# Optimization experiments

Measured on AMD Instinct MI355X. Metric: run time of the kernel, lower is better.

## Reference

```python
import jax, jax.numpy as jnp
import numpy as np

TOP_K = 2


def setup_inputs() -> dict:
    key = jax.random.key(0)
    ks = jax.random.split(key, 8)
    B, S, H, I, E = 1, 1024, 2048, 1408, 8
    s = 0.02  # init scale for weights
    return {
        "hidden_states": jax.random.normal(ks[0], (B, S, H), jnp.float32),
        "gate_weight": jax.random.normal(ks[1], (E, H), jnp.float32) * s,
        "expert_gate_w": jax.random.normal(ks[2], (E, I, H), jnp.float32) * s,
        "expert_up_w": jax.random.normal(ks[3], (E, I, H), jnp.float32) * s,
        "expert_down_w": jax.random.normal(ks[4], (E, H, I), jnp.float32) * s,
        "shared_gate_w": jax.random.normal(ks[5], (I, H), jnp.float32) * s,
        "shared_up_w": jax.random.normal(ks[6], (I, H), jnp.float32) * s,
        "shared_down_w": jax.random.normal(ks[7], (H, I), jnp.float32) * s,
    }


def reference(hidden_states, gate_weight, expert_gate_w, expert_up_w, expert_down_w,
              shared_gate_w, shared_up_w, shared_down_w):
    B, S, H = hidden_states.shape
    E = gate_weight.shape[0]
    x = hidden_states.reshape(-1, H)          # [T, H]
    T = x.shape[0]

    # --- gate: top-k routing (e_score_correction_bias buffer is zeros -> no-op) ---
    logits = x @ gate_weight.T                # [T, E]
    topk_logits, topk_idx = jax.lax.top_k(logits, TOP_K)
    topk_w = jax.nn.softmax(topk_logits, axis=-1)  # [T, K]

    # per-token per-expert combine weight (0 for non-selected experts) [T, E]
    comb = jnp.zeros((T, E), x.dtype).at[jnp.arange(T)[:, None], topk_idx].add(topk_w)

    # --- routed experts: dense over E, weighted combine (mathematically identical
    # to the per-token loop since comb==0 for unselected experts) ---
    g = jnp.einsum('th,eih->tei', x, expert_gate_w)   # [T, E, I]
    u = jnp.einsum('th,eih->tei', x, expert_up_w)     # [T, E, I]
    h = jax.nn.silu(g) * u                            # [T, E, I]
    y = jnp.einsum('tei,ehi->teh', h, expert_down_w)  # [T, E, H]
    out = jnp.einsum('teh,te->th', y, comb)           # [T, H]

    # --- shared expert ---
    sh = (jax.nn.silu(x @ shared_gate_w.T) * (x @ shared_up_w.T)) @ shared_down_w.T
    out = out + sh
    return out.reshape(B, S, H)
```

## Files before the change

### kernel.cpp

```cpp
#include <hip/hip_runtime.h>
#include <hip/hip_bf16.h>

typedef unsigned short u16;
typedef __bf16 bf16x8 __attribute__((ext_vector_type(8)));
typedef float f32x4 __attribute__((ext_vector_type(4)));

#define H_DIM 2048
#define I_DIM 1408
#define T_TOK 1024
#define NEXP 8
#define LS 40

__device__ __forceinline__ u16 f2bf(float f) {
    union { float f; unsigned u; } v; v.f = f;
    unsigned r = v.u + 0x7FFFu + ((v.u >> 16) & 1u);
    return (u16)(r >> 16);
}
__device__ __forceinline__ unsigned pack2(float a, float b) {
    float2 t; t.x = a; t.y = b;
    __hip_bfloat162 h = __float22bfloat162_rn(t);
    union { __hip_bfloat162 h; unsigned u; } v; v.h = h;
    return v.u;
}
__device__ __forceinline__ uint2 pack4(float4 f) {
    uint2 r; r.x = pack2(f.x, f.y); r.y = pack2(f.z, f.w); return r;
}
__device__ __forceinline__ void g2l16(const void* g, void* l) {
    __builtin_amdgcn_global_load_lds((const __attribute__((address_space(1))) void*)g,
                                     (__attribute__((address_space(3))) void*)l, 16, 0, 0);
}

__global__ __launch_bounds__(256)
void router_kernel(const float* __restrict__ x, const float* __restrict__ gw,
                   int* __restrict__ counts, int* __restrict__ tok, float* __restrict__ tw) {
    int wave = threadIdx.x >> 6;
    int lane = threadIdx.x & 63;
    int t = blockIdx.x * 4 + wave;
    const float* xr = x + (size_t)t * H_DIM;
    float acc[NEXP];
#pragma unroll
    for (int e = 0; e < NEXP; e++) acc[e] = 0.f;
    for (int h = lane; h < H_DIM; h += 64) {
        float xv = xr[h];
#pragma unroll
        for (int e = 0; e < NEXP; e++) acc[e] += xv * gw[e * H_DIM + h];
    }
#pragma unroll
    for (int e = 0; e < NEXP; e++) {
#pragma unroll
        for (int off = 32; off > 0; off >>= 1) acc[e] += __shfl_xor(acc[e], off);
    }
    if (lane == 0) {
        int i0 = 0; float v0 = acc[0];
#pragma unroll
        for (int e = 1; e < NEXP; e++) if (acc[e] > v0) { v0 = acc[e]; i0 = e; }
        int i1 = -1; float v1 = -3.0e38f;
#pragma unroll
        for (int e = 0; e < NEXP; e++) if (e != i0 && acc[e] > v1) { v1 = acc[e]; i1 = e; }
        float ex = __expf(v1 - v0);
        float w0 = 1.f / (1.f + ex);
        float w1 = 1.f - w0;
        int s0 = atomicAdd(&counts[i0], 1);
        tok[i0 * T_TOK + s0] = t; tw[i0 * T_TOK + s0] = w0;
        int s1 = atomicAdd(&counts[i1], 1);
        tok[i1 * T_TOK + s1] = t; tw[i1 * T_TOK + s1] = w1;
    }
}

struct Cvt7 { const float* in[7]; u16* out[7]; int nchunk[7]; };
__global__ __launch_bounds__(256)
void convert_bf(Cvt7 a) {
    int z = blockIdx.z;
    int n = a.nchunk[z];
    const float* in = a.in[z]; u16* out = a.out[z];
    for (int i = blockIdx.x * 256 + threadIdx.x; i < n; i += gridDim.x * 256) {
        const float4* p = (const float4*)(in + (size_t)i * 8);
        float4 f0 = p[0], f1 = p[1];
        uint4 o; o.x = pack2(f0.x, f0.y); o.y = pack2(f0.z, f0.w);
        o.z = pack2(f1.x, f1.y); o.w = pack2(f1.z, f1.w);
        *(uint4*)(out + (size_t)i * 8) = o;
    }
}

__global__ __launch_bounds__(256, 3)
void gate_up_bf(const u16* __restrict__ xb,
                const u16* __restrict__ egw, const u16* __restrict__ euw,
                const u16* __restrict__ sgw, const u16* __restrict__ suw,
                const int* __restrict__ counts, const int* __restrict__ tok,
                const float* __restrict__ tw,
                u16* __restrict__ h_r, u16* __restrict__ h_s) {
    __shared__ u16 lA[64 * 64];
    __shared__ u16 lG[128 * 64];
    __shared__ u16 lU[128 * 64];

    int e = blockIdx.z;
    bool routed = (e < NEXP);
    int cnt, hbase; const u16 *Wg, *Wu; u16* hout;
    if (routed) {
        cnt = counts[e];
        int p = 0;
#pragma unroll
        for (int i = 0; i < NEXP; i++) { int c = counts[i]; if (i < e) p += c; }
        hbase = p;
        Wg = egw + (size_t)e * I_DIM * H_DIM;
        Wu = euw + (size_t)e * I_DIM * H_DIM;
        hout = h_r;
    } else { cnt = T_TOK; hbase = 0; Wg = sgw; Wu = suw; hout = h_s; }
    int m0 = blockIdx.y * 64;
    if (m0 >= cnt) return;
    int n0 = blockIdx.x * 128;

    int tid = threadIdx.x, lane = tid & 63, w = tid >> 6;

    const u16* aptr[2]; u16* alds[2];
#pragma unroll
    for (int j = 0; j < 2; j++) {
        int chunk = w * 128 + j * 64 + lane;
        int row = chunk >> 3, cl = chunk & 7;
        int cg = cl ^ (row & 7);
        int trow = m0 + row; if (trow > cnt - 1) trow = cnt - 1;
        int tix = routed ? tok[e * T_TOK + trow] : trow;
        aptr[j] = xb + (size_t)tix * H_DIM + cg * 8;
        alds[j] = &lA[(w * 128 + j * 64) * 8];
    }
    const u16* gptr[4]; const u16* uptr[4]; u16* glds[4]; u16* ulds[4];
#pragma unroll
    for (int j = 0; j < 4; j++) {
        int chunk = w * 256 + j * 64 + lane;
        int row = chunk >> 3, cl = chunk & 7;
        int cg = cl ^ (row & 7);
        gptr[j] = Wg + (size_t)(n0 + row) * H_DIM + cg * 8;
        uptr[j] = Wu + (size_t)(n0 + row) * H_DIM + cg * 8;
        glds[j] = &lG[(w * 256 + j * 64) * 8];
        ulds[j] = &lU[(w * 256 + j * 64) * 8];
    }

    f32x4 zero = {0.f, 0.f, 0.f, 0.f};
    f32x4 accg[4][2], accu[4][2];
#pragma unroll
    for (int a = 0; a < 4; a++)
#pragma unroll
        for (int b = 0; b < 2; b++) { accg[a][b] = zero; accu[a][b] = zero; }

    int r16 = lane & 15, q = lane >> 4;

    for (int k0 = 0; k0 < H_DIM; k0 += 64) {
#pragma unroll
        for (int j = 0; j < 2; j++) g2l16(aptr[j] + k0, alds[j]);
#pragma unroll
        for (int j = 0; j < 4; j++) { g2l16(gptr[j] + k0, glds[j]); g2l16(uptr[j] + k0, ulds[j]); }
        __syncthreads();
#pragma unroll
        for (int kh = 0; kh < 2; kh++) {
            bf16x8 af[4], gf[2], uf[2];
#pragma unroll
            for (int mi = 0; mi < 4; mi++) {
                int row = mi * 16 + r16;
                int ch = (kh * 4 + q) ^ (row & 7);
                af[mi] = *(const bf16x8*)&lA[row * 64 + ch * 8];
            }
#pragma unroll
            for (int ni = 0; ni < 2; ni++) {
                int row = w * 32 + ni * 16 + r16;
                int ch = (kh * 4 + q) ^ (row & 7);
                gf[ni] = *(const bf16x8*)&lG[row * 64 + ch * 8];
                uf[ni] = *(const bf16x8*)&lU[row * 64 + ch * 8];
            }
#pragma unroll
            for (int mi = 0; mi < 4; mi++)
#pragma unroll
                for (int ni = 0; ni < 2; ni++) {
                    accg[mi][ni] = __builtin_amdgcn_mfma_f32_16x16x32_bf16(af[mi], gf[ni], accg[mi][ni], 0, 0, 0);
                    accu[mi][ni] = __builtin_amdgcn_mfma_f32_16x16x32_bf16(af[mi], uf[ni], accu[mi][ni], 0, 0, 0);
                }
        }
        __syncthreads();
    }

#pragma unroll
    for (int mi = 0; mi < 4; mi++) {
#pragma unroll
        for (int r = 0; r < 4; r++) {
            int row = mi * 16 + q * 4 + r;
            int gr = m0 + row;
            if (gr < cnt) {
                float wt = routed ? tw[e * T_TOK + gr] : 1.0f;
                u16* hrow = hout + (size_t)(hbase + gr) * I_DIM + n0 + w * 32;
#pragma unroll
                for (int ni = 0; ni < 2; ni++) {
                    float g = accg[mi][ni][r], u = accu[mi][ni][r];
                    float hv = (g / (1.f + __expf(-g))) * u * wt;
                    hrow[ni * 16 + r16] = f2bf(hv);
                }
            }
        }
    }
}

__global__ __launch_bounds__(256, 3)
void down_bf(const u16* __restrict__ h_r, const u16* __restrict__ h_s,
             const u16* __restrict__ edw, const u16* __restrict__ sdw,
             const int* __restrict__ counts, const int* __restrict__ tok,
             float* __restrict__ out) {
    __shared__ u16 lA[64 * 64];
    __shared__ u16 lB[128 * 64];

    int e = blockIdx.z;
    bool routed = (e < NEXP);
    int cnt, hbase; const u16* Wd; const u16* hin;
    if (routed) {
        cnt = counts[e];
        int p = 0;
#pragma unroll
        for (int i = 0; i < NEXP; i++) { int c = counts[i]; if (i < e) p += c; }
        hbase = p;
        Wd = edw + (size_t)e * H_DIM * I_DIM;
        hin = h_r;
    } else { cnt = T_TOK; hbase = 0; Wd = sdw; hin = h_s; }
    int m0 = blockIdx.y * 64;
    if (m0 >= cnt) return;
    int n0 = blockIdx.x * 128;

    int tid = threadIdx.x, lane = tid & 63, w = tid >> 6;

    const u16* aptr[2]; u16* alds[2];
#pragma unroll
    for (int j = 0; j < 2; j++) {
        int chunk = w * 128 + j * 64 + lane;
        int row = chunk >> 3, cl = chunk & 7;
        int cg = cl ^ (row & 7);
        int hr = m0 + row; if (hr > cnt - 1) hr = cnt - 1;
        aptr[j] = hin + (size_t)(hbase + hr) * I_DIM + cg * 8;
        alds[j] = &lA[(w * 128 + j * 64) * 8];
    }
    const u16* bptr[4]; u16* blds[4];
#pragma unroll
    for (int j = 0; j < 4; j++) {
        int chunk = w * 256 + j * 64 + lane;
        int row = chunk >> 3, cl = chunk & 7;
        int cg = cl ^ (row & 7);
        bptr[j] = Wd + (size_t)(n0 + row) * I_DIM + cg * 8;
        blds[j] = &lB[(w * 256 + j * 64) * 8];
    }

    f32x4 zero = {0.f, 0.f, 0.f, 0.f};
    f32x4 acc[4][2];
#pragma unroll
    for (int a = 0; a < 4; a++)
#pragma unroll
        for (int b = 0; b < 2; b++) acc[a][b] = zero;

    int r16 = lane & 15, q = lane >> 4;

    for (int k0 = 0; k0 < I_DIM; k0 += 64) {
#pragma unroll
        for (int j = 0; j < 2; j++) g2l16(aptr[j] + k0, alds[j]);
#pragma unroll
        for (int j = 0; j < 4; j++) g2l16(bptr[j] + k0, blds[j]);
        __syncthreads();
#pragma unroll
        for (int kh = 0; kh < 2; kh++) {
            bf16x8 af[4], bfr[2];
#pragma unroll
            for (int mi = 0; mi < 4; mi++) {
                int row = mi * 16 + r16;
                int ch = (kh * 4 + q) ^ (row & 7);
                af[mi] = *(const bf16x8*)&lA[row * 64 + ch * 8];
            }
#pragma unroll
            for (int ni = 0; ni < 2; ni++) {
                int row = w * 32 + ni * 16 + r16;
                int ch = (kh * 4 + q) ^ (row & 7);
                bfr[ni] = *(const bf16x8*)&lB[row * 64 + ch * 8];
            }
#pragma unroll
            for (int mi = 0; mi < 4; mi++)
#pragma unroll
                for (int ni = 0; ni < 2; ni++)
                    acc[mi][ni] = __builtin_amdgcn_mfma_f32_16x16x32_bf16(af[mi], bfr[ni], acc[mi][ni], 0, 0, 0);
        }
        __syncthreads();
    }

#pragma unroll
    for (int mi = 0; mi < 4; mi++) {
#pragma unroll
        for (int r = 0; r < 4; r++) {
            int row = mi * 16 + q * 4 + r;
            int gr = m0 + row;
            if (gr < cnt) {
                int t = routed ? tok[e * T_TOK + gr] : gr;
                float* orow = out + (size_t)t * H_DIM + n0 + w * 32;
#pragma unroll
                for (int ni = 0; ni < 2; ni++)
                    atomicAdd(&orow[ni * 16 + r16], acc[mi][ni][r]);
            }
        }
    }
}

__global__ __launch_bounds__(256, 2)
void gate_up_f32(const float* __restrict__ x,
                 const float* __restrict__ egw, const float* __restrict__ euw,
                 const float* __restrict__ sgw, const float* __restrict__ suw,
                 const int* __restrict__ counts, const int* __restrict__ tok,
                 const float* __restrict__ tw,
                 u16* __restrict__ h_r, u16* __restrict__ h_s) {
    __shared__ u16 lA[64 * LS];
    __shared__ u16 lG[128 * LS];
    __shared__ u16 lU[128 * LS];
    int e = blockIdx.z;
    bool routed = (e < NEXP);
    int cnt, hbase; const float *Wg, *Wu; u16* hout;
    if (routed) {
        cnt = counts[e];
        int p = 0;
#pragma unroll
        for (int i = 0; i < NEXP; i++) { int c = counts[i]; if (i < e) p += c; }
        hbase = p;
        Wg = egw + (size_t)e * I_DIM * H_DIM; Wu = euw + (size_t)e * I_DIM * H_DIM; hout = h_r;
    } else { cnt = T_TOK; hbase = 0; Wg = sgw; Wu = suw; hout = h_s; }
    int m0 = blockIdx.y * 64;
    if (m0 >= cnt) return;
    int n0 = blockIdx.x * 128;
    int tid = threadIdx.x, lane = tid & 63, w = tid >> 6;
    const float* ap[2]; int sa[2];
#pragma unroll
    for (int i = 0; i < 2; i++) {
        int slot = tid + i * 256;
        int row = slot >> 3, c4 = slot & 7;
        sa[i] = row * LS + c4 * 4;
        int trow = m0 + row; if (trow > cnt - 1) trow = cnt - 1;
        int tix = routed ? tok[e * T_TOK + trow] : trow;
        ap[i] = x + (size_t)tix * H_DIM + c4 * 4;
    }
    const float* gp[4]; const float* up[4]; int sg[4];
#pragma unroll
    for (int i = 0; i < 4; i++) {
        int slot = tid + i * 256;
        int row = slot >> 3, c4 = slot & 7;
        sg[i] = row * LS + c4 * 4;
        gp[i] = Wg + (size_t)(n0 + row) * H_DIM + c4 * 4;
        up[i] = Wu + (size_t)(n0 + row) * H_DIM + c4 * 4;
    }
    f32x4 zero = {0.f, 0.f, 0.f, 0.f};
    f32x4 accg[4][2], accu[4][2];
#pragma unroll
    for (int a = 0; a < 4; a++)
#pragma unroll
        for (int b = 0; b < 2; b++) { accg[a][b] = zero; accu[a][b] = zero; }
    int r16 = lane & 15, kq = lane >> 4;
    float4 ra[2], rg[4], ru[4];
#pragma unroll
    for (int i = 0; i < 2; i++) ra[i] = *(const float4*)(ap[i]);
#pragma unroll
    for (int i = 0; i < 4; i++) { rg[i] = *(const float4*)(gp[i]); ru[i] = *(const float4*)(up[i]); }
    for (int k0 = 0; k0 < H_DIM; k0 += 32) {
#pragma unroll
        for (int i = 0; i < 2; i++) *(uint2*)&lA[sa[i]] = pack4(ra[i]);
#pragma unroll
        for (int i = 0; i < 4; i++) { *(uint2*)&lG[sg[i]] = pack4(rg[i]); *(uint2*)&lU[sg[i]] = pack4(ru[i]); }
        __syncthreads();
        if (k0 + 32 < H_DIM) {
            int kn = k0 + 32;
#pragma unroll
            for (int i = 0; i < 2; i++) ra[i] = *(const float4*)(ap[i] + kn);
#pragma unroll
            for (int i = 0; i < 4; i++) { rg[i] = *(const float4*)(gp[i] + kn); ru[i] = *(const float4*)(up[i] + kn); }
        }
        bf16x8 af[4], gf[2], uf[2];
#pragma unroll
        for (int mi = 0; mi < 4; mi++) af[mi] = *(const bf16x8*)&lA[(mi * 16 + r16) * LS + kq * 8];
#pragma unroll
        for (int ni = 0; ni < 2; ni++) {
            gf[ni] = *(const bf16x8*)&lG[(w * 32 + ni * 16 + r16) * LS + kq * 8];
            uf[ni] = *(const bf16x8*)&lU[(w * 32 + ni * 16 + r16) * LS + kq * 8];
        }
#pragma unroll
        for (int mi = 0; mi < 4; mi++)
#pragma unroll
            for (int ni = 0; ni < 2; ni++) {
                accg[mi][ni] = __builtin_amdgcn_mfma_f32_16x16x32_bf16(af[mi], gf[ni], accg[mi][ni], 0, 0, 0);
                accu[mi][ni] = __builtin_amdgcn_mfma_f32_16x16x32_bf16(af[mi], uf[ni], accu[mi][ni], 0, 0, 0);
            }
        __syncthreads();
    }
#pragma unroll
    for (int mi = 0; mi < 4; mi++) {
#pragma unroll
        for (int r = 0; r < 4; r++) {
            int row = mi * 16 + kq * 4 + r;
            int gr = m0 + row;
            if (gr < cnt) {
                float wt = routed ? tw[e * T_TOK + gr] : 1.0f;
                u16* hrow = hout + (size_t)(hbase + gr) * I_DIM + n0 + w * 32;
#pragma unroll
                for (int ni = 0; ni < 2; ni++) {
                    float g = accg[mi][ni][r], u = accu[mi][ni][r];
                    float hv = (g / (1.f + __expf(-g))) * u * wt;
                    hrow[ni * 16 + r16] = f2bf(hv);
                }
            }
        }
    }
}

__global__ __launch_bounds__(256, 2)
void down_f32(const u16* __restrict__ h_r, const u16* __restrict__ h_s,
              const float* __restrict__ edw, const float* __restrict__ sdw,
              const int* __restrict__ counts, const int* __restrict__ tok,
              float* __restrict__ out) {
    __shared__ u16 lA[64 * LS];
    __shared__ u16 lB[128 * LS];
    int e = blockIdx.z;
    bool routed = (e < NEXP);
    int cnt, hbase; const float* Wd; const u16* hin;
    if (routed) {
        cnt = counts[e];
        int p = 0;
#pragma unroll
        for (int i = 0; i < NEXP; i++) { int c = counts[i]; if (i < e) p += c; }
        hbase = p;
        Wd = edw + (size_t)e * H_DIM * I_DIM; hin = h_r;
    } else { cnt = T_TOK; hbase = 0; Wd = sdw; hin = h_s; }
    int m0 = blockIdx.y * 64;
    if (m0 >= cnt) return;
    int n0 = blockIdx.x * 128;
    int tid = threadIdx.x, lane = tid & 63, w = tid >> 6;
    int arow = tid >> 2, ac8 = tid & 3;
    int hr = m0 + arow; if (hr > cnt - 1) hr = cnt - 1;
    const u16* ap = hin + (size_t)(hbase + hr) * I_DIM + ac8 * 8;
    int sa = arow * LS + ac8 * 8;
    const float* bp[4]; int sb[4];
#pragma unroll
    for (int i = 0; i < 4; i++) {
        int slot = tid + i * 256;
        int row = slot >> 3, c4 = slot & 7;
        bp[i] = Wd + (size_t)(n0 + row) * I_DIM + c4 * 4;
        sb[i] = row * LS + c4 * 4;
    }
    f32x4 zero = {0.f, 0.f, 0.f, 0.f};
    f32x4 acc[4][2];
#pragma unroll
    for (int a = 0; a < 4; a++)
#pragma unroll
        for (int b = 0; b < 2; b++) acc[a][b] = zero;
    int r16 = lane & 15, kq = lane >> 4;
    uint4 ra = *(const uint4*)(ap);
    float4 rb[4];
#pragma unroll
    for (int i = 0; i < 4; i++) rb[i] = *(const float4*)(bp[i]);
    for (int k0 = 0; k0 < I_DIM; k0 += 32) {
        *(uint4*)&lA[sa] = ra;
#pragma unroll
        for (int i = 0; i < 4; i++) *(uint2*)&lB[sb[i]] = pack4(rb[i]);
        __syncthreads();
        if (k0 + 32 < I_DIM) {
            int kn = k0 + 32;
            ra = *(const uint4*)(ap + kn);
#pragma unroll
            for (int i = 0; i < 4; i++) rb[i] = *(const float4*)(bp[i] + kn);
        }
        bf16x8 af[4], bfr[2];
#pragma unroll
        for (int mi = 0; mi < 4; mi++) af[mi] = *(const bf16x8*)&lA[(mi * 16 + r16) * LS + kq * 8];
#pragma unroll
        for (int ni = 0; ni < 2; ni++) bfr[ni] = *(const bf16x8*)&lB[(w * 32 + ni * 16 + r16) * LS + kq * 8];
#pragma unroll
        for (int mi = 0; mi < 4; mi++)
#pragma unroll
            for (int ni = 0; ni < 2; ni++)
                acc[mi][ni] = __builtin_amdgcn_mfma_f32_16x16x32_bf16(af[mi], bfr[ni], acc[mi][ni], 0, 0, 0);
        __syncthreads();
    }
#pragma unroll
    for (int mi = 0; mi < 4; mi++) {
#pragma unroll
        for (int r = 0; r < 4; r++) {
            int row = mi * 16 + kq * 4 + r;
            int gr = m0 + row;
            if (gr < cnt) {
                int t = routed ? tok[e * T_TOK + gr] : gr;
                float* orow = out + (size_t)t * H_DIM + n0 + w * 32;
#pragma unroll
                for (int ni = 0; ni < 2; ni++)
                    atomicAdd(&orow[ni * 16 + r16], acc[mi][ni][r]);
            }
        }
    }
}

extern "C" void kernel_launch(void* const* d_in, const int* in_sizes, int n_in,
                              void* d_out, int out_size, void* d_ws, size_t ws_size,
                              hipStream_t stream) {
    const float* x   = (const float*)d_in[0];
    const float* gw  = (const float*)d_in[1];
    const float* egw = (const float*)d_in[2];
    const float* euw = (const float*)d_in[3];
    const float* edw = (const float*)d_in[4];
    const float* sgw = (const float*)d_in[5];
    const float* suw = (const float*)d_in[6];
    const float* sdw = (const float*)d_in[7];
    float* out = (float*)d_out;

    char* ws = (char*)d_ws;
    int*   counts = (int*)ws;
    int*   tok    = (int*)(ws + 256);
    float* tw     = (float*)(ws + 256 + 32768);
    u16*   h_r    = (u16*)(ws + 65792);
    u16*   h_s    = h_r + (size_t)2048 * I_DIM;

    hipMemsetAsync(counts, 0, 32, stream);
    hipMemsetAsync(out, 0, (size_t)T_TOK * H_DIM * sizeof(float), stream);
    router_kernel<<<256, 256, 0, stream>>>(x, gw, counts, tok, tw);

    const size_t NEED = 168624384ull;
    if (ws_size >= NEED) {
        u16* xbf = (u16*)(ws + 8716544);
        u16* egb = (u16*)(ws + 12910848);
        u16* eub = (u16*)(ws + 59048192);
        u16* edb = (u16*)(ws + 105185536);
        u16* sgb = (u16*)(ws + 151322880);
        u16* sub = (u16*)(ws + 157090048);
        u16* sdb = (u16*)(ws + 162857216);
        Cvt7 c;
        c.in[0] = egw; c.out[0] = egb; c.nchunk[0] = 2883584;
        c.in[1] = euw; c.out[1] = eub; c.nchunk[1] = 2883584;
        c.in[2] = edw; c.out[2] = edb; c.nchunk[2] = 2883584;
        c.in[3] = sgw; c.out[3] = sgb; c.nchunk[3] = 360448;
        c.in[4] = suw; c.out[4] = sub; c.nchunk[4] = 360448;
        c.in[5] = sdw; c.out[5] = sdb; c.nchunk[5] = 360448;
        c.in[6] = x;   c.out[6] = xbf; c.nchunk[6] = 262144;
        convert_bf<<<dim3(2048, 1, 7), 256, 0, stream>>>(c);
        gate_up_bf<<<dim3(11, 16, 9), 256, 0, stream>>>(xbf, egb, eub, sgb, sub, counts, tok, tw, h_r, h_s);
        down_bf<<<dim3(16, 16, 9), 256, 0, stream>>>(h_r, h_s, edb, sdb, counts, tok, out);
    } else {
        gate_up_f32<<<dim3(11, 16, 9), 256, 0, stream>>>(x, egw, euw, sgw, suw, counts, tok, tw, h_r, h_s);
        down_f32<<<dim3(16, 16, 9), 256, 0, stream>>>(h_r, h_s, edw, sdw, counts, tok, out);
    }
}
```

Baseline: 523.7 us.

## Fuse router into weight-conversion prep, enlarge GEMM warp tiles, replace atomics with reduce

```diff
diff --git a/kernel.cpp b/kernel.cpp
--- a/kernel.cpp
+++ b/kernel.cpp
@@ -28,6 +28,309 @@
 __device__ __forceinline__ void g2l16(const void* g, void* l) {
     __builtin_amdgcn_global_load_lds((const __attribute__((address_space(1))) void*)g,
                                      (__attribute__((address_space(3))) void*)l, 16, 0, 0);
+}
+
+struct PrepArgs {
+    const float* cin[6]; u16* cout[6]; int n16[6];
+    const float* x; const float* gw; u16* xb;
+    int* counts; int* tok; float* tw; unsigned* tslot;
+};
+
+__global__ __launch_bounds__(256)
+void prep_kernel(PrepArgs a) {
+    int z = blockIdx.z;
+    if (z < 6) {
+        int n = a.n16[z];
+        const float4* in = (const float4*)a.cin[z];
+        uint4* out = (uint4*)a.cout[z];
+        for (int i = blockIdx.x * 256 + threadIdx.x; i < n; i += gridDim.x * 256) {
+            const float4* p = in + (size_t)i * 4;
+            float4 f0 = p[0], f1 = p[1], f2 = p[2], f3 = p[3];
+            uint4 o0, o1;
+            o0.x = pack2(f0.x, f0.y); o0.y = pack2(f0.z, f0.w);
+            o0.z = pack2(f1.x, f1.y); o0.w = pack2(f1.z, f1.w);
+            o1.x = pack2(f2.x, f2.y); o1.y = pack2(f2.z, f2.w);
+            o1.z = pack2(f3.x, f3.y); o1.w = pack2(f3.z, f3.w);
+            out[(size_t)i * 2]     = o0;
+            out[(size_t)i * 2 + 1] = o1;
+        }
+    } else {
+        if (blockIdx.x >= 256) return;
+        int wave = threadIdx.x >> 6, lane = threadIdx.x & 63;
+        int t = blockIdx.x * 4 + wave;
+        const float4* xr = (const float4*)(a.x + (size_t)t * H_DIM);
+        const float4* gw4 = (const float4*)a.gw;
+        uint2* xbr = (uint2*)(a.xb + (size_t)t * H_DIM);
+        float acc[NEXP];
+#pragma unroll
+        for (int e = 0; e < NEXP; e++) acc[e] = 0.f;
+#pragma unroll
+        for (int j = 0; j < 8; j++) {
+            int c = lane + j * 64;
+            float4 xv = xr[c];
+            xbr[c] = pack4(xv);
+#pragma unroll
+            for (int e = 0; e < NEXP; e++) {
+                float4 gv = gw4[e * 512 + c];
+                acc[e] += xv.x * gv.x + xv.y * gv.y + xv.z * gv.z + xv.w * gv.w;
+            }
+        }
+#pragma unroll
+        for (int e = 0; e < NEXP; e++) {
+#pragma unroll
+            for (int off = 32; off > 0; off >>= 1) acc[e] += __shfl_xor(acc[e], off);
+        }
+        if (lane == 0) {
+            int i0 = 0; float v0 = acc[0];
+#pragma unroll
+            for (int e = 1; e < NEXP; e++) if (acc[e] > v0) { v0 = acc[e]; i0 = e; }
+            int i1 = -1; float v1 = -3.0e38f;
+#pragma unroll
+            for (int e = 0; e < NEXP; e++) if (e != i0 && acc[e] > v1) { v1 = acc[e]; i1 = e; }
+            float ex = __expf(v1 - v0);
+            float w0 = 1.f / (1.f + ex);
+            float w1 = 1.f - w0;
+            int s0 = atomicAdd(&a.counts[i0], 1);
+            a.tok[i0 * T_TOK + s0] = t; a.tw[i0 * T_TOK + s0] = w0;
+            a.tslot[t * 2] = ((unsigned)i0 << 16) | (unsigned)s0;
+            int s1 = atomicAdd(&a.counts[i1], 1);
+            a.tok[i1 * T_TOK + s1] = t; a.tw[i1 * T_TOK + s1] = w1;
+            a.tslot[t * 2 + 1] = ((unsigned)i1 << 16) | (unsigned)s1;
+        }
+    }
+}
+
+__global__ __launch_bounds__(128, 2)
+void gate_up_bf(const u16* __restrict__ xb,
+                const u16* __restrict__ egb, const u16* __restrict__ eub,
+                const u16* __restrict__ sgb, const u16* __restrict__ sub,
+                const int* __restrict__ counts, const int* __restrict__ tok,
+                const float* __restrict__ tw,
+                u16* __restrict__ h_r, u16* __restrict__ h_s) {
+    __shared__ u16 lA[64 * 64];
+    __shared__ u16 lG[128 * 64];
+    __shared__ u16 lU[128 * 64];
+
+    int e = blockIdx.z;
+    bool routed = (e < NEXP);
+    int cnt, hbase; const u16 *Wg, *Wu; u16* hout;
+    if (routed) {
+        cnt = counts[e];
+        int p = 0;
+#pragma unroll
+        for (int i = 0; i < NEXP; i++) { int c = counts[i]; if (i < e) p += c; }
+        hbase = p;
+        Wg = egb + (size_t)e * I_DIM * H_DIM;
+        Wu = eub + (size_t)e * I_DIM * H_DIM;
+        hout = h_r;
+    } else { cnt = T_TOK; hbase = 0; Wg = sgb; Wu = sub; hout = h_s; }
+    int m0 = blockIdx.y * 64;
+    if (m0 >= cnt) return;
+    int n0 = blockIdx.x * 128;
+
+    int tid = threadIdx.x, lane = tid & 63, w = tid >> 6;
+    int l3 = lane >> 3, cl = lane & 7;
+    int cg = cl ^ l3;
+
+    const u16* aptr[4];
+#pragma unroll
+    for (int j = 0; j < 4; j++) {
+        int row = w * 32 + j * 8 + l3;
+        int trow = m0 + row; if (trow > cnt - 1) trow = cnt - 1;
+        int tix = routed ? tok[e * T_TOK + trow] : trow;
+        aptr[j] = xb + (size_t)tix * H_DIM + cg * 8;
+    }
+    const u16* gbase = Wg + (size_t)(n0 + w * 64 + l3) * H_DIM + cg * 8;
+    const u16* ubase = Wu + (size_t)(n0 + w * 64 + l3) * H_DIM + cg * 8;
+
+    u16* aldsb = &lA[w * 2048];
+    u16* gldsb = &lG[w * 4096];
+    u16* uldsb = &lU[w * 4096];
+
+    f32x4 zero = {0.f, 0.f, 0.f, 0.f};
+    f32x4 accg[4][4], accu[4][4];
+#pragma unroll
+    for (int a = 0; a < 4; a++)
+#pragma unroll
+        for (int b = 0; b < 4; b++) { accg[a][b] = zero; accu[a][b] = zero; }
+
+    int r16 = lane & 15, q = lane >> 4;
+
+    for (int k0 = 0; k0 < H_DIM; k0 += 64) {
+#pragma unroll
+        for (int j = 0; j < 4; j++) g2l16(aptr[j] + k0, aldsb + j * 512);
+#pragma unroll
+        for (int j = 0; j < 8; j++) {
+            g2l16(gbase + (size_t)j * 8 * H_DIM + k0, gldsb + j * 512);
+            g2l16(ubase + (size_t)j * 8 * H_DIM + k0, uldsb + j * 512);
+        }
+        __syncthreads();
+#pragma unroll
+        for (int kh = 0; kh < 2; kh++) {
+            bf16x8 af[4], gf[4], uf[4];
+#pragma unroll
+            for (int mi = 0; mi < 4; mi++) {
+                int row = mi * 16 + r16;
+                int ch = (kh * 4 + q) ^ (row & 7);
+                af[mi] = *(const bf16x8*)&lA[row * 64 + ch * 8];
+            }
+#pragma unroll
+            for (int ni = 0; ni < 4; ni++) {
+                int row = w * 64 + ni * 16 + r16;
+                int ch = (kh * 4 + q) ^ (row & 7);
+                gf[ni] = *(const bf16x8*)&lG[row * 64 + ch * 8];
+                uf[ni] = *(const bf16x8*)&lU[row * 64 + ch * 8];
+            }
+#pragma unroll
+            for (int mi = 0; mi < 4; mi++)
+#pragma unroll
+                for (int ni = 0; ni < 4; ni++) {
+                    accg[mi][ni] = __builtin_amdgcn_mfma_f32_16x16x32_bf16(af[mi], gf[ni], accg[mi][ni], 0, 0, 0);
+                    accu[mi][ni] = __builtin_amdgcn_mfma_f32_16x16x32_bf16(af[mi], uf[ni], accu[mi][ni], 0, 0, 0);
+                }
+        }
+        __syncthreads();
+    }
+
+#pragma unroll
+    for (int mi = 0; mi < 4; mi++) {
+#pragma unroll
+        for (int r = 0; r < 4; r++) {
+            int row = mi * 16 + q * 4 + r;
+            int gr = m0 + row;
+            if (gr < cnt) {
+                float wt = routed ? tw[e * T_TOK + gr] : 1.0f;
+                u16* hrow = hout + (size_t)(hbase + gr) * I_DIM + n0 + w * 64;
+#pragma unroll
+                for (int ni = 0; ni < 4; ni++) {
+                    float g = accg[mi][ni][r], u = accu[mi][ni][r];
+                    hrow[ni * 16 + r16] = f2bf((g / (1.f + __expf(-g))) * u * wt);
+                }
+            }
+        }
+    }
+}
+
+__global__ __launch_bounds__(128, 2)
+void down_bf(const u16* __restrict__ h_r, const u16* __restrict__ h_s,
+             const u16* __restrict__ edb, const u16* __restrict__ sdb,
+             const int* __restrict__ counts, const int* __restrict__ tok,
+             float* __restrict__ y_r, float* __restrict__ y_s) {
+    __shared__ u16 lA[64 * 64];
+    __shared__ u16 lB[128 * 64];
+
+    int e = blockIdx.z;
+    bool routed = (e < NEXP);
+    int cnt, hbase; const u16* Wd; const u16* hin;
+    if (routed) {
+        cnt = counts[e];
+        int p = 0;
+#pragma unroll
+        for (int i = 0; i < NEXP; i++) { int c = counts[i]; if (i < e) p += c; }
+        hbase = p;
+        Wd = edb + (size_t)e * H_DIM * I_DIM;
+        hin = h_r;
+    } else { cnt = T_TOK; hbase = 0; Wd = sdb; hin = h_s; }
+    int m0 = blockIdx.y * 64;
+    if (m0 >= cnt) return;
+    int n0 = blockIdx.x * 128;
+
+    int tid = threadIdx.x, lane = tid & 63, w = tid >> 6;
+    int l3 = lane >> 3, cl = lane & 7;
+    int cg = cl ^ l3;
+
+    const u16* aptr[4];
+#pragma unroll
+    for (int j = 0; j < 4; j++) {
+        int row = w * 32 + j * 8 + l3;
+        int hr = m0 + row; if (hr > cnt - 1) hr = cnt - 1;
+        aptr[j] = hin + (size_t)(hbase + hr) * I_DIM + cg * 8;
+    }
+    const u16* bbase = Wd + (size_t)(n0 + w * 64 + l3) * I_DIM + cg * 8;
+
+    u16* aldsb = &lA[w * 2048];
+    u16* bldsb = &lB[w * 4096];
+
+    f32x4 zero = {0.f, 0.f, 0.f, 0.f};
+    f32x4 acc[4][4];
+#pragma unroll
+    for (int a = 0; a < 4; a++)
+#pragma unroll
+        for (int b = 0; b < 4; b++) acc[a][b] = zero;
+
+    int r16 = lane & 15, q = lane >> 4;
+
+    for (int k0 = 0; k0 < I_DIM; k0 += 64) {
+#pragma unroll
+        for (int j = 0; j < 4; j++) g2l16(aptr[j] + k0, aldsb + j * 512);
+#pragma unroll
+        for (int j = 0; j < 8; j++) g2l16(bbase + (size_t)j * 8 * I_DIM + k0, bldsb + j * 512);
+        __syncthreads();
+#pragma unroll
+        for (int kh = 0; kh < 2; kh++) {
+            bf16x8 af[4], bfr[4];
+#pragma unroll
+            for (int mi = 0; mi < 4; mi++) {
+                int row = mi * 16 + r16;
+                int ch = (kh * 4 + q) ^ (row & 7);
+                af[mi] = *(const bf16x8*)&lA[row * 64 + ch * 8];
+            }
+#pragma unroll
+            for (int ni = 0; ni < 4; ni++) {
+                int row = w * 64 + ni * 16 + r16;
+                int ch = (kh * 4 + q) ^ (row & 7);
+                bfr[ni] = *(const bf16x8*)&lB[row * 64 + ch * 8];
+            }
+#pragma unroll
+            for (int mi = 0; mi < 4; mi++)
+#pragma unroll
+                for (int ni = 0; ni < 4; ni++)
+                    acc[mi][ni] = __builtin_amdgcn_mfma_f32_16x16x32_bf16(af[mi], bfr[ni], acc[mi][ni], 0, 0, 0);
+        }
+        __syncthreads();
+    }
+
+#pragma unroll
+    for (int mi = 0; mi < 4; mi++) {
+#pragma unroll
+        for (int r = 0; r < 4; r++) {
+            int row = mi * 16 + q * 4 + r;
+            int gr = m0 + row;
+            if (gr < cnt) {
+                float* yrow = (routed ? y_r + (size_t)(hbase + gr) * H_DIM
+                                      : y_s + (size_t)gr * H_DIM) + n0 + w * 64;
+#pragma unroll
+                for (int ni = 0; ni < 4; ni++)
+                    yrow[ni * 16 + r16] = acc[mi][ni][r];
+            }
+        }
+    }
+}
+
+__global__ __launch_bounds__(256)
+void reduce_kernel(const int* __restrict__ counts, const unsigned* __restrict__ tslot,
+                   const float* __restrict__ y_r, const float* __restrict__ y_s,
+                   float* __restrict__ out) {
+    int t = blockIdx.x;
+    int pre[NEXP]; int run = 0;
+#pragma unroll
+    for (int i = 0; i < NEXP; i++) { pre[i] = run; run += counts[i]; }
+    unsigned t0 = tslot[t * 2], t1 = tslot[t * 2 + 1];
+    int r0 = pre[t0 >> 16] + (int)(t0 & 0xffffu);
+    int r1 = pre[t1 >> 16] + (int)(t1 & 0xffffu);
+    const float4* ys = (const float4*)(y_s + (size_t)t * H_DIM);
+    const float4* a0 = (const float4*)(y_r + (size_t)r0 * H_DIM);
+    const float4* a1 = (const float4*)(y_r + (size_t)r1 * H_DIM);
+    float4* o = (float4*)(out + (size_t)t * H_DIM);
+#pragma unroll
+    for (int j = 0; j < 2; j++) {
+        int c = threadIdx.x + j * 256;
+        float4 s = ys[c], b0 = a0[c], b1 = a1[c];
+        float4 r;
+        r.x = s.x + b0.x + b1.x; r.y = s.y + b0.y + b1.y;
+        r.z = s.z + b0.z + b1.z; r.w = s.w + b0.w + b1.w;
+        o[c] = r;
+    }
 }
 
 __global__ __launch_bounds__(256)
@@ -64,238 +367,6 @@
         tok[i0 * T_TOK + s0] = t; tw[i0 * T_TOK + s0] = w0;
         int s1 = atomicAdd(&counts[i1], 1);
         tok[i1 * T_TOK + s1] = t; tw[i1 * T_TOK + s1] = w1;
-    }
-}
-
-struct Cvt7 { const float* in[7]; u16* out[7]; int nchunk[7]; };
-__global__ __launch_bounds__(256)
-void convert_bf(Cvt7 a) {
-    int z = blockIdx.z;
-    int n = a.nchunk[z];
-    const float* in = a.in[z]; u16* out = a.out[z];
-    for (int i = blockIdx.x * 256 + threadIdx.x; i < n; i += gridDim.x * 256) {
-        const float4* p = (const float4*)(in + (size_t)i * 8);
-        float4 f0 = p[0], f1 = p[1];
-        uint4 o; o.x = pack2(f0.x, f0.y); o.y = pack2(f0.z, f0.w);
-        o.z = pack2(f1.x, f1.y); o.w = pack2(f1.z, f1.w);
-        *(uint4*)(out + (size_t)i * 8) = o;
-    }
-}
-
-__global__ __launch_bounds__(256, 3)
-void gate_up_bf(const u16* __restrict__ xb,
-                const u16* __restrict__ egw, const u16* __restrict__ euw,
-                const u16* __restrict__ sgw, const u16* __restrict__ suw,
-                const int* __restrict__ counts, const int* __restrict__ tok,
-                const float* __restrict__ tw,
-                u16* __restrict__ h_r, u16* __restrict__ h_s) {
-    __shared__ u16 lA[64 * 64];
-    __shared__ u16 lG[128 * 64];
-    __shared__ u16 lU[128 * 64];
-
-    int e = blockIdx.z;
-    bool routed = (e < NEXP);
-    int cnt, hbase; const u16 *Wg, *Wu; u16* hout;
-    if (routed) {
-        cnt = counts[e];
-        int p = 0;
-#pragma unroll
-        for (int i = 0; i < NEXP; i++) { int c = counts[i]; if (i < e) p += c; }
-        hbase = p;
-        Wg = egw + (size_t)e * I_DIM * H_DIM;
-        Wu = euw + (size_t)e * I_DIM * H_DIM;
-        hout = h_r;
-    } else { cnt = T_TOK; hbase = 0; Wg = sgw; Wu = suw; hout = h_s; }
-    int m0 = blockIdx.y * 64;
-    if (m0 >= cnt) return;
-    int n0 = blockIdx.x * 128;
-
-    int tid = threadIdx.x, lane = tid & 63, w = tid >> 6;
-
-    const u16* aptr[2]; u16* alds[2];
-#pragma unroll
-    for (int j = 0; j < 2; j++) {
-        int chunk = w * 128 + j * 64 + lane;
-        int row = chunk >> 3, cl = chunk & 7;
-        int cg = cl ^ (row & 7);
-        int trow = m0 + row; if (trow > cnt - 1) trow = cnt - 1;
-        int tix = routed ? tok[e * T_TOK + trow] : trow;
-        aptr[j] = xb + (size_t)tix * H_DIM + cg * 8;
-        alds[j] = &lA[(w * 128 + j * 64) * 8];
-    }
-    const u16* gptr[4]; const u16* uptr[4]; u16* glds[4]; u16* ulds[4];
-#pragma unroll
-    for (int j = 0; j < 4; j++) {
-        int chunk = w * 256 + j * 64 + lane;
-        int row = chunk >> 3, cl = chunk & 7;
-        int cg = cl ^ (row & 7);
-        gptr[j] = Wg + (size_t)(n0 + row) * H_DIM + cg * 8;
-        uptr[j] = Wu + (size_t)(n0 + row) * H_DIM + cg * 8;
-        glds[j] = &lG[(w * 256 + j * 64) * 8];
-        ulds[j] = &lU[(w * 256 + j * 64) * 8];
-    }
-
-    f32x4 zero = {0.f, 0.f, 0.f, 0.f};
-    f32x4 accg[4][2], accu[4][2];
-#pragma unroll
-    for (int a = 0; a < 4; a++)
-#pragma unroll
-        for (int b = 0; b < 2; b++) { accg[a][b] = zero; accu[a][b] = zero; }
-
-    int r16 = lane & 15, q = lane >> 4;
-
-    for (int k0 = 0; k0 < H_DIM; k0 += 64) {
-#pragma unroll
-        for (int j = 0; j < 2; j++) g2l16(aptr[j] + k0, alds[j]);
-#pragma unroll
-        for (int j = 0; j < 4; j++) { g2l16(gptr[j] + k0, glds[j]); g2l16(uptr[j] + k0, ulds[j]); }
-        __syncthreads();
-#pragma unroll
-        for (int kh = 0; kh < 2; kh++) {
-            bf16x8 af[4], gf[2], uf[2];
-#pragma unroll
-            for (int mi = 0; mi < 4; mi++) {
-                int row = mi * 16 + r16;
-                int ch = (kh * 4 + q) ^ (row & 7);
-                af[mi] = *(const bf16x8*)&lA[row * 64 + ch * 8];
-            }
-#pragma unroll
-            for (int ni = 0; ni < 2; ni++) {
-                int row = w * 32 + ni * 16 + r16;
-                int ch = (kh * 4 + q) ^ (row & 7);
-                gf[ni] = *(const bf16x8*)&lG[row * 64 + ch * 8];
-                uf[ni] = *(const bf16x8*)&lU[row * 64 + ch * 8];
-            }
-#pragma unroll
-            for (int mi = 0; mi < 4; mi++)
-#pragma unroll
-                for (int ni = 0; ni < 2; ni++) {
-                    accg[mi][ni] = __builtin_amdgcn_mfma_f32_16x16x32_bf16(af[mi], gf[ni], accg[mi][ni], 0, 0, 0);
-                    accu[mi][ni] = __builtin_amdgcn_mfma_f32_16x16x32_bf16(af[mi], uf[ni], accu[mi][ni], 0, 0, 0);
-                }
-        }
-        __syncthreads();
-    }
-
-#pragma unroll
-    for (int mi = 0; mi < 4; mi++) {
-#pragma unroll
-        for (int r = 0; r < 4; r++) {
-            int row = mi * 16 + q * 4 + r;
-            int gr = m0 + row;
-            if (gr < cnt) {
-                float wt = routed ? tw[e * T_TOK + gr] : 1.0f;
-                u16* hrow = hout + (size_t)(hbase + gr) * I_DIM + n0 + w * 32;
-#pragma unroll
-                for (int ni = 0; ni < 2; ni++) {
-                    float g = accg[mi][ni][r], u = accu[mi][ni][r];
-                    float hv = (g / (1.f + __expf(-g))) * u * wt;
-                    hrow[ni * 16 + r16] = f2bf(hv);
-                }
-            }
-        }
-    }
-}
-
-__global__ __launch_bounds__(256, 3)
-void down_bf(const u16* __restrict__ h_r, const u16* __restrict__ h_s,
-             const u16* __restrict__ edw, const u16* __restrict__ sdw,
-             const int* __restrict__ counts, const int* __restrict__ tok,
-             float* __restrict__ out) {
-    __shared__ u16 lA[64 * 64];
-    __shared__ u16 lB[128 * 64];
-
-    int e = blockIdx.z;
-    bool routed = (e < NEXP);
-    int cnt, hbase; const u16* Wd; const u16* hin;
-    if (routed) {
-        cnt = counts[e];
-        int p = 0;
-#pragma unroll
-        for (int i = 0; i < NEXP; i++) { int c = counts[i]; if (i < e) p += c; }
-        hbase = p;
-        Wd = edw + (size_t)e * H_DIM * I_DIM;
-        hin = h_r;
-    } else { cnt = T_TOK; hbase = 0; Wd = sdw; hin = h_s; }
-    int m0 = blockIdx.y * 64;
-    if (m0 >= cnt) return;
-    int n0 = blockIdx.x * 128;
-
-    int tid = threadIdx.x, lane = tid & 63, w = tid >> 6;
-
-    const u16* aptr[2]; u16* alds[2];
-#pragma unroll
-    for (int j = 0; j < 2; j++) {
-        int chunk = w * 128 + j * 64 + lane;
-        int row = chunk >> 3, cl = chunk & 7;
-        int cg = cl ^ (row & 7);
-        int hr = m0 + row; if (hr > cnt - 1) hr = cnt - 1;
-        aptr[j] = hin + (size_t)(hbase + hr) * I_DIM + cg * 8;
-        alds[j] = &lA[(w * 128 + j * 64) * 8];
-    }
-    const u16* bptr[4]; u16* blds[4];
-#pragma unroll
-    for (int j = 0; j < 4; j++) {
-        int chunk = w * 256 + j * 64 + lane;
-        int row = chunk >> 3, cl = chunk & 7;
-        int cg = cl ^ (row & 7);
-        bptr[j] = Wd + (size_t)(n0 + row) * I_DIM + cg * 8;
-        blds[j] = &lB[(w * 256 + j * 64) * 8];
-    }
-
-    f32x4 zero = {0.f, 0.f, 0.f, 0.f};
-    f32x4 acc[4][2];
-#pragma unroll
-    for (int a = 0; a < 4; a++)
-#pragma unroll
-        for (int b = 0; b < 2; b++) acc[a][b] = zero;
-
-    int r16 = lane & 15, q = lane >> 4;
-
-    for (int k0 = 0; k0 < I_DIM; k0 += 64) {
-#pragma unroll
-        for (int j = 0; j < 2; j++) g2l16(aptr[j] + k0, alds[j]);
-#pragma unroll
-        for (int j = 0; j < 4; j++) g2l16(bptr[j] + k0, blds[j]);
-        __syncthreads();
-#pragma unroll
-        for (int kh = 0; kh < 2; kh++) {
-            bf16x8 af[4], bfr[2];
-#pragma unroll
-            for (int mi = 0; mi < 4; mi++) {
-                int row = mi * 16 + r16;
-                int ch = (kh * 4 + q) ^ (row & 7);
-                af[mi] = *(const bf16x8*)&lA[row * 64 + ch * 8];
-            }
-#pragma unroll
-            for (int ni = 0; ni < 2; ni++) {
-                int row = w * 32 + ni * 16 + r16;
-                int ch = (kh * 4 + q) ^ (row & 7);
-                bfr[ni] = *(const bf16x8*)&lB[row * 64 + ch * 8];
-            }
-#pragma unroll
-            for (int mi = 0; mi < 4; mi++)
-#pragma unroll
-                for (int ni = 0; ni < 2; ni++)
-                    acc[mi][ni] = __builtin_amdgcn_mfma_f32_16x16x32_bf16(af[mi], bfr[ni], acc[mi][ni], 0, 0, 0);
-        }
-        __syncthreads();
-    }
-
-#pragma unroll
-    for (int mi = 0; mi < 4; mi++) {
-#pragma unroll
-        for (int r = 0; r < 4; r++) {
-            int row = mi * 16 + q * 4 + r;
-            int gr = m0 + row;
-            if (gr < cnt) {
-                int t = routed ? tok[e * T_TOK + gr] : gr;
-                float* orow = out + (size_t)t * H_DIM + n0 + w * 32;
-#pragma unroll
-                for (int ni = 0; ni < 2; ni++)
-                    atomicAdd(&orow[ni * 16 + r16], acc[mi][ni][r]);
-            }
-        }
     }
 }
 
@@ -397,8 +468,7 @@
 #pragma unroll
                 for (int ni = 0; ni < 2; ni++) {
                     float g = accg[mi][ni][r], u = accu[mi][ni][r];
-                    float hv = (g / (1.f + __expf(-g))) * u * wt;
-                    hrow[ni * 16 + r16] = f2bf(hv);
+                    hrow[ni * 16 + r16] = f2bf((g / (1.f + __expf(-g))) * u * wt);
                 }
             }
         }
@@ -504,37 +574,42 @@
     float* out = (float*)d_out;
 
     char* ws = (char*)d_ws;
-    int*   counts = (int*)ws;
-    int*   tok    = (int*)(ws + 256);
-    float* tw     = (float*)(ws + 256 + 32768);
-    u16*   h_r    = (u16*)(ws + 65792);
-    u16*   h_s    = h_r + (size_t)2048 * I_DIM;
+    int*      counts = (int*)ws;
+    int*      tok    = (int*)(ws + 256);
+    float*    tw     = (float*)(ws + 33024);
+    unsigned* tslot  = (unsigned*)(ws + 65792);
+    u16*      h_r    = (u16*)(ws + 73984);
+    u16*      h_s    = (u16*)(ws + 5841152);
+    u16*      xb     = (u16*)(ws + 8724736);
+    u16*      egb    = (u16*)(ws + 12919040);
+    u16*      eub    = (u16*)(ws + 59056384);
+    u16*      edb    = (u16*)(ws + 105193728);
+    u16*      sgb    = (u16*)(ws + 151331072);
+    u16*      sub    = (u16*)(ws + 157098240);
+    u16*      sdb    = (u16*)(ws + 162865408);
+    float*    y_r    = (float*)(ws + 12919040);
+    float*    y_s    = (float*)(ws + 29696256);
 
     hipMemsetAsync(counts, 0, 32, stream);
-    hipMemsetAsync(out, 0, (size_t)T_TOK * H_DIM * sizeof(float), stream);
-    router_kernel<<<256, 256, 0, stream>>>(x, gw, counts, tok, tw);
-
-    const size_t NEED = 168624384ull;
+
+    const size_t NEED = 168632576ull;
     if (ws_size >= NEED) {
-        u16* xbf = (u16*)(ws + 8716544);
-        u16* egb = (u16*)(ws + 12910848);
-        u16* eub = (u16*)(ws + 59048192);
-        u16* edb = (u16*)(ws + 105185536);
-        u16* sgb = (u16*)(ws + 151322880);
-        u16* sub = (u16*)(ws + 157090048);
-        u16* sdb = (u16*)(ws + 162857216);
-        Cvt7 c;
-        c.in[0] = egw; c.out[0] = egb; c.nchunk[0] = 2883584;
-        c.in[1] = euw; c.out[1] = eub; c.nchunk[1] = 2883584;
-        c.in[2] = edw; c.out[2] = edb; c.nchunk[2] = 2883584;
-        c.in[3] = sgw; c.out[3] = sgb; c.nchunk[3] = 360448;
-        c.in[4] = suw; c.out[4] = sub; c.nchunk[4] = 360448;
-        c.in[5] = sdw; c.out[5] = sdb; c.nchunk[5] = 360448;
-        c.in[6] = x;   c.out[6] = xbf; c.nchunk[6] = 262144;
-        convert_bf<<<dim3(2048, 1, 7), 256, 0, stream>>>(c);
-        gate_up_bf<<<dim3(11, 16, 9), 256, 0, stream>>>(xbf, egb, eub, sgb, sub, counts, tok, tw, h_r, h_s);
-        down_bf<<<dim3(16, 16, 9), 256, 0, stream>>>(h_r, h_s, edb, sdb, counts, tok, out);
+        PrepArgs pa;
+        pa.cin[0] = egw; pa.cout[0] = egb; pa.n16[0] = 1441792;
+        pa.cin[1] = euw; pa.cout[1] = eub; pa.n16[1] = 1441792;
+        pa.cin[2] = edw; pa.cout[2] = edb; pa.n16[2] = 1441792;
+        pa.cin[3] = sgw; pa.cout[3] = sgb; pa.n16[3] = 180224;
+        pa.cin[4] = suw; pa.cout[4] = sub; pa.n16[4] = 180224;
+        pa.cin[5] = sdw; pa.cout[5] = sdb; pa.n16[5] = 180224;
+        pa.x = x; pa.gw = gw; pa.xb = xb;
+        pa.counts = counts; pa.tok = tok; pa.tw = tw; pa.tslot = tslot;
+        prep_kernel<<<dim3(1024, 1, 7), 256, 0, stream>>>(pa);
+        gate_up_bf<<<dim3(11, 16, 9), 128, 0, stream>>>(xb, egb, eub, sgb, sub, counts, tok, tw, h_r, h_s);
+        down_bf<<<dim3(16, 16, 9), 128, 0, stream>>>(h_r, h_s, edb, sdb, counts, tok, y_r, y_s);
+        reduce_kernel<<<1024, 256, 0, stream>>>(counts, tslot, y_r, y_s, out);
     } else {
+        hipMemsetAsync(out, 0, (size_t)T_TOK * H_DIM * sizeof(float), stream);
+        router_kernel<<<256, 256, 0, stream>>>(x, gw, counts, tok, tw);
         gate_up_f32<<<dim3(11, 16, 9), 256, 0, stream>>>(x, egw, euw, sgw, suw, counts, tok, tw, h_r, h_s);
         down_f32<<<dim3(16, 16, 9), 256, 0, stream>>>(h_r, h_s, edw, sdw, counts, tok, out);
     }
```

Measured after the change: 504.0 us. -3.8%, faster.
